# Kernel optimization log

Measured on AMD Instinct MI355X. Metric: run time of the kernel, lower is better.

## Reference

```python
import jax, jax.numpy as jnp
import numpy as np

B, M, N, P, H, W, D, DIMG, NH = 32, 2048, 512, 16, 640, 640, 256, 384, 8
PD = 3 * P * P  # 768 flattened patch dim


def layer_norm(x, g, b, eps=1e-5):
    mu = x.mean(-1, keepdims=True)
    var = ((x - mu) ** 2).mean(-1, keepdims=True)
    return (x - mu) * jax.lax.rsqrt(var + eps) * g + b


def get_patches(img, kpts, patch):
    # img [B,3,H,W], kpts [B,N,2] (x,y), NaN rows -> NaN patches
    Bb, C, Hh, Ww = img.shape
    half = patch // 2
    safe = jnp.nan_to_num(kpts, nan=0.0)
    ctr = jnp.round(safe).astype(jnp.int32)
    x0 = jnp.clip(ctr[..., 0] - half, 0, Ww - patch)
    y0 = jnp.clip(ctr[..., 1] - half, 0, Hh - patch)
    offs = jnp.arange(patch)
    ys = y0[..., None] + offs  # [B,N,P]
    xs = x0[..., None] + offs  # [B,N,P]

    def ext(im_b, ys_b, xs_b):
        p = im_b[:, ys_b[:, :, None], xs_b[:, None, :]]  # [C,N,P,P]
        return jnp.transpose(p, (1, 0, 2, 3))  # [N,C,P,P]

    patches = jax.vmap(ext)(img, ys, xs)  # [B,N,C,P,P]
    invalid = jnp.isnan(kpts).any(-1)
    return jnp.where(invalid[:, :, None, None, None], jnp.nan, patches)


def setup_inputs() -> dict:
    key = jax.random.key(0)
    ks = jax.random.split(key, 16)
    im0 = jax.random.uniform(ks[0], (B, 3, H, W), jnp.float32)
    im1 = jax.random.uniform(ks[1], (B, 3, H, W), jnp.float32)
    wh = jnp.array([W - 1.0, H - 1.0], jnp.float32)
    kpts0 = jax.random.uniform(ks[2], (B, M, 2), jnp.float32) * wh
    kpts1 = jax.random.uniform(ks[3], (B, M, 2), jnp.float32) * wh
    scores0 = jax.random.uniform(ks[4], (B, M), jnp.float32)
    scores1 = jax.random.uniform(ks[5], (B, M), jnp.float32)
    image_embs = jax.random.normal(ks[6], (B, DIMG), jnp.float32)
    m0 = jax.random.randint(ks[7], (B, N), 0, M)
    m1 = jax.random.randint(ks[8], (B, N), -300, M)
    m1 = jnp.where(m1 < 0, -1, m1)
    sorted_matches = jnp.stack([m0, m1], axis=-1).astype(jnp.int32)
    s = 0.02
    params = dict(
        ln1_g=jnp.ones((PD,), jnp.float32), ln1_b=jnp.zeros((PD,), jnp.float32),
        W_pe=jax.random.normal(ks[9], (D - 1, PD), jnp.float32) * s,
        b_pe=jnp.zeros((D - 1,), jnp.float32),
        ln2_g=jnp.ones((D - 1,), jnp.float32), ln2_b=jnp.zeros((D - 1,), jnp.float32),
        W_proj=jax.random.normal(ks[10], (D, DIMG), jnp.float32) * s,
        b_proj=jnp.zeros((D,), jnp.float32),
        in_w=jax.random.normal(ks[11], (3 * D, D), jnp.float32) * s,
        in_b=jnp.zeros((3 * D,), jnp.float32),
        out_w=jax.random.normal(ks[12], (D, D), jnp.float32) * s,
        out_b=jnp.zeros((D,), jnp.float32),
        W_fc=jax.random.normal(ks[13], (6, D), jnp.float32) * s,
        b_fc=jnp.zeros((6,), jnp.float32),
    )
    return dict(im0=im0, im1=im1, kpts0=kpts0, kpts1=kpts1, scores0=scores0,
                scores1=scores1, image_embs=image_embs,
                sorted_matches=sorted_matches, **params)


def reference(im0, im1, kpts0, kpts1, scores0, scores1, image_embs,
              sorted_matches, ln1_g, ln1_b, W_pe, b_pe, ln2_g, ln2_b,
              W_proj, b_proj, in_w, in_b, out_w, out_b, W_fc, b_fc):
    im0 = jnp.clip(im0, 0.0, 1.0)
    im1 = jnp.clip(im1, 0.0, 1.0)
    m0 = sorted_matches[..., 0]
    m1 = sorted_matches[..., 1]
    valid = m1 > -1  # [B,N]
    m0c = jnp.clip(m0, 0, M - 1)
    m1c = jnp.clip(m1, 0, M - 1)
    # vectorized masked gather with NaN padding (replaces the double python loop)
    g0 = jnp.take_along_axis(kpts0, m0c[..., None], axis=1)  # [B,N,2]
    g1 = jnp.take_along_axis(kpts1, m1c[..., None], axis=1)
    k0v = jnp.where(valid[..., None], g0, jnp.nan)
    k1v = jnp.where(valid[..., None], g1, jnp.nan)
    s0v = jnp.where(valid, jnp.take_along_axis(scores0, m0c, axis=1), 0.0)
    s1v = jnp.where(valid, jnp.take_along_axis(scores1, m1c, axis=1), 0.0)
    p0 = jnp.nan_to_num(get_patches(im0, k0v, P), nan=-1.0)  # [B,N,3,P,P]
    p1 = jnp.nan_to_num(get_patches(im1, k1v, P), nan=-1.0)
    patches = jnp.concatenate([p0, p1], axis=1)  # [B,2N,3,P,P]
    flat = patches.reshape(B, 2 * N, PD)
    e = layer_norm(flat, ln1_g, ln1_b)
    e = e @ W_pe.T + b_pe
    e = layer_norm(e, ln2_g, ln2_b)  # [B,2N,D-1]
    scores = jnp.concatenate([s0v, s1v], axis=1)  # [B,2N]
    pe = jnp.concatenate([e, scores[..., None]], axis=-1)  # [B,2N,D]
    # motion estimator: cross-attn, query = projected image embedding
    q = image_embs @ W_proj.T + b_proj  # [B,D]
    Wq, Wk, Wv = in_w[:D], in_w[D:2 * D], in_w[2 * D:]
    bq, bk, bv = in_b[:D], in_b[D:2 * D], in_b[2 * D:]
    dh = D // NH
    qh = (q @ Wq.T + bq).reshape(B, 1, NH, dh)
    kh = (pe @ Wk.T + bk).reshape(B, 2 * N, NH, dh)
    vh = (pe @ Wv.T + bv).reshape(B, 2 * N, NH, dh)
    scale = 1.0 / np.sqrt(dh).astype(np.float32)
    att = jnp.einsum('bqhd,bkhd->bhqk', qh, kh) * scale
    a = jax.nn.softmax(att, axis=-1)
    o = jnp.einsum('bhqk,bkhd->bqhd', a, vh).reshape(B, 1, D)
    o = o @ out_w.T + out_b
    out = (o @ W_fc.T + b_fc).reshape(B, 6)
    return out
```

## Files before the change

### kernel.cpp

```cpp
#include <hip/hip_runtime.h>
#include <math.h>

#define BB 32
#define MM 2048
#define NN 512
#define PSZ 16
#define HH 640
#define WW 640
#define DD 256
#define DIMG_ 384
#define NHEADS 8
#define PD_ 768
#define TWO_N 1024
#define ROWS_TOT (BB * TWO_N)
#define CHCT 32

typedef short bf16x8 __attribute__((ext_vector_type(8)));
typedef float f32x4  __attribute__((ext_vector_type(4)));

__device__ __forceinline__ unsigned short f2bf(float x) {
  unsigned int u = __float_as_uint(x);
  u = (u + 0x7FFF + ((u >> 16) & 1)) >> 16;
  return (unsigned short)u;
}
__device__ __forceinline__ float bf2f(unsigned short h) {
  return __uint_as_float(((unsigned int)h) << 16);
}

__device__ __forceinline__ void gload_lds16(const void* g, void* l) {
  __builtin_amdgcn_global_load_lds(
      (const __attribute__((address_space(1))) void*)g,
      (__attribute__((address_space(3))) void*)l, 16, 0, 0);
}

__global__ __launch_bounds__(256) void prep_extract_kernel(
    const float* __restrict__ W_pe,
    unsigned short* __restrict__ Whi, unsigned short* __restrict__ Wlo,
    const float* __restrict__ image_embs,
    const float* __restrict__ W_proj, const float* __restrict__ b_proj,
    const float* __restrict__ in_w,   const float* __restrict__ in_b,
    float* __restrict__ u_out, float* __restrict__ bias_out,
    const float* __restrict__ im0, const float* __restrict__ im1,
    const float* __restrict__ kpts0, const float* __restrict__ kpts1,
    const float* __restrict__ scores0, const float* __restrict__ scores1,
    const int*   __restrict__ sorted_matches,
    const float* __restrict__ ln1_g, const float* __restrict__ ln1_b,
    unsigned short* __restrict__ Ahi, unsigned short* __restrict__ Alo,
    float* __restrict__ score_all)
{
  __shared__ float q1[DD];
  __shared__ float q2[DD];
  const int t = threadIdx.x;

  if (blockIdx.x < 768) {
    const int idx = blockIdx.x * 256 + t;
    const int row = idx / PD_;
    float v = (row < 255) ? W_pe[idx] : 0.0f;
    const unsigned short h = f2bf(v);
    Whi[idx] = h;
    Wlo[idx] = f2bf(v - bf2f(h));
    return;
  }

  if (blockIdx.x < 800) {
    const int b = blockIdx.x - 768;
    {
      const float4* emb = (const float4*)(image_embs + (size_t)b * DIMG_);
      const float4* wr  = (const float4*)(W_proj + (size_t)t * DIMG_);
      float a = b_proj[t];
      #pragma unroll 4
      for (int i = 0; i < DIMG_ / 4; ++i) {
        const float4 e4 = emb[i], w4 = wr[i];
        a += e4.x * w4.x + e4.y * w4.y + e4.z * w4.z + e4.w * w4.w;
      }
      q1[t] = a;
    }
    __syncthreads();
    {
      const float4* wr = (const float4*)(in_w + (size_t)t * DD);
      const float4* qq = (const float4*)q1;
      float a = in_b[t];
      #pragma unroll 4
      for (int i = 0; i < DD / 4; ++i) {
        const float4 q4 = qq[i], w4 = wr[i];
        a += q4.x * w4.x + q4.y * w4.y + q4.z * w4.z + q4.w * w4.w;
      }
      q2[t] = a;
    }
    __syncthreads();
    #pragma unroll
    for (int h = 0; h < NHEADS; ++h) {
      float s = 0.0f;
      #pragma unroll 8
      for (int i = 0; i < 32; ++i)
        s += q2[h * 32 + i] * in_w[(size_t)(DD + h * 32 + i) * DD + t];
      u_out[((size_t)b * NHEADS + h) * DD + t] = s;
    }
    if (t < NHEADS) {
      float s = 0.0f;
      for (int i = 0; i < 32; ++i) s += q2[t * 32 + i] * in_b[DD + t * 32 + i];
      bias_out[b * NHEADS + t] = s;
    }
    return;
  }

  const int L  = t & 63;
  const long gp = (long)(blockIdx.x - 800) * 4 + (t >> 6);
  const int b   = (int)(gp >> 10);
  const int n2  = (int)(gp & 1023);
  const bool side1 = (n2 >= NN);
  const float* img  = side1 ? im1 : im0;
  const float* kpts = side1 ? kpts1 : kpts0;
  const float* scrs = side1 ? scores1 : scores0;

  const int n  = side1 ? (n2 - NN) : n2;
  const int m0 = sorted_matches[((size_t)b * NN + n) * 2 + 0];
  const int m1 = sorted_matches[((size_t)b * NN + n) * 2 + 1];
  const bool valid = (m1 > -1);
  int midx = side1 ? m1 : m0;
  midx = min(max(midx, 0), MM - 1);
  const float kx = kpts[((size_t)b * MM + midx) * 2 + 0];
  const float ky = kpts[((size_t)b * MM + midx) * 2 + 1];
  const int x0 = min(max((int)rintf(kx) - 8, 0), WW - PSZ);
  const int y0 = min(max((int)rintf(ky) - 8, 0), HH - PSZ);

  float v[12];
  if (valid) {
    const size_t imb = (size_t)b * 3 * HH * WW;
    const int px = (2 * L) & 15;
    #pragma unroll
    for (int j = 0; j < 6; ++j) {
      const int p0 = 2 * L + 128 * j;
      const int c  = p0 >> 8;
      const int py = (p0 >> 4) & 15;
      const float* rp = img + imb + ((size_t)c * HH + y0 + py) * WW + x0 + px;
      v[2 * j]     = fminf(fmaxf(rp[0], 0.0f), 1.0f);
      v[2 * j + 1] = fminf(fmaxf(rp[1], 0.0f), 1.0f);
    }
  } else {
    #pragma unroll
    for (int i = 0; i < 12; ++i) v[i] = -1.0f;
  }

  float s = 0.0f, ss = 0.0f;
  #pragma unroll
  for (int i = 0; i < 12; ++i) { s += v[i]; ss += v[i] * v[i]; }
  #pragma unroll
  for (int m = 32; m; m >>= 1) { s += __shfl_xor(s, m); ss += __shfl_xor(ss, m); }
  const float mu  = s * (1.0f / 768.0f);
  const float var = ss * (1.0f / 768.0f) - mu * mu;
  const float rs  = 1.0f / sqrtf(var + 1e-5f);

  unsigned int* AhiW = (unsigned int*)(Ahi + gp * PD_);
  unsigned int* AloW = (unsigned int*)(Alo + gp * PD_);
  #pragma unroll
  for (int j = 0; j < 6; ++j) {
    const int p0 = 2 * L + 128 * j;
    const float y0e = (v[2 * j]     - mu) * rs * ln1_g[p0]     + ln1_b[p0];
    const float y1e = (v[2 * j + 1] - mu) * rs * ln1_g[p0 + 1] + ln1_b[p0 + 1];
    const unsigned short h0 = f2bf(y0e), h1 = f2bf(y1e);
    AhiW[p0 >> 1] = (unsigned int)h0 | ((unsigned int)h1 << 16);
    const unsigned short l0 = f2bf(y0e - bf2f(h0));
    const unsigned short l1 = f2bf(y1e - bf2f(h1));
    AloW[p0 >> 1] = (unsigned int)l0 | ((unsigned int)l1 << 16);
  }
  if (L == 0) {
    score_all[gp] = valid ? scrs[(size_t)b * MM + midx] : 0.0f;
  }
}

__global__ __launch_bounds__(256, 2) void gemm_fused_kernel(
    const unsigned short* __restrict__ Ahi, const unsigned short* __restrict__ Alo,
    const unsigned short* __restrict__ Whi, const unsigned short* __restrict__ Wlo,
    const float* __restrict__ b_pe,
    const float* __restrict__ ln2_g, const float* __restrict__ ln2_b,
    const float* __restrict__ score_all,
    float* __restrict__ pe)
{
  __shared__ __align__(16) unsigned short sm[20480];
  const int t = threadIdx.x;
  const int w = t >> 6, L = t & 63;
  const int mt = blockIdx.x;

  const int rr   = L >> 2;
  const int q_st = (L & 3) ^ ((L >> 4) & 3);
  const int lane_m = L & 15, quad = L >> 4;
  const int swz = quad ^ (lane_m >> 2);

  const unsigned short* gsrc[10];
  int ldst[10];
  #pragma unroll
  for (int c = 0; c < 10; ++c) {
    const int cc = w + 4 * c;
    const unsigned short* sp; long rb; int dst;
    if (cc < 4)       { sp = Ahi; rb = (long)mt * 64 + cc * 16;       dst = cc * 512; }
    else if (cc < 8)  { sp = Alo; rb = (long)mt * 64 + (cc - 4) * 16; dst = 2048 + (cc - 4) * 512; }
    else if (cc < 24) { sp = Whi; rb = (long)(cc - 8) * 16;           dst = 4096 + (cc - 8) * 512; }
    else              { sp = Wlo; rb = (long)(cc - 24) * 16;          dst = 12288 + (cc - 24) * 512; }
    gsrc[c] = sp + (rb + rr) * (long)PD_ + q_st * 8;
    ldst[c] = dst;
  }

  f32x4 acc[4][4];
  #pragma unroll
  for (int i = 0; i < 4; ++i)
    #pragma unroll
    for (int j = 0; j < 4; ++j) acc[i][j] = (f32x4){0.f, 0.f, 0.f, 0.f};

  for (int ks = 0; ks < PD_ / 32; ++ks) {
    const int k0 = ks * 32;
    __syncthreads();
    #pragma unroll
    for (int c = 0; c < 10; ++c)
      gload_lds16(gsrc[c] + k0, sm + ldst[c]);
    __syncthreads();

    bf16x8 ah[4], al[4];
    #pragma unroll
    for (int i = 0; i < 4; ++i) {
      const int offa = (i * 16 + lane_m) * 32 + swz * 8;
      ah[i] = *(const bf16x8*)(sm + offa);
      al[i] = *(const bf16x8*)(sm + 2048 + offa);
    }
    #pragma unroll
    for (int j = 0; j < 4; ++j) {
      const int offb = (w * 64 + j * 16 + lane_m) * 32 + swz * 8;
      const bf16x8 bh = *(const bf16x8*)(sm + 4096 + offb);
      const bf16x8 bl = *(const bf16x8*)(sm + 12288 + offb);
      #pragma unroll
      for (int i = 0; i < 4; ++i) {
        acc[i][j] = __builtin_amdgcn_mfma_f32_16x16x32_bf16(ah[i], bh, acc[i][j], 0, 0, 0);
        acc[i][j] = __builtin_amdgcn_mfma_f32_16x16x32_bf16(ah[i], bl, acc[i][j], 0, 0, 0);
        acc[i][j] = __builtin_amdgcn_mfma_f32_16x16x32_bf16(al[i], bh, acc[i][j], 0, 0, 0);
      }
    }
  }

  __syncthreads();
  float* const fs = (float*)sm;
  float p4[4], g4[4], b4[4];
  #pragma unroll
  for (int j = 0; j < 4; ++j) {
    const int c = w * 64 + j * 16 + lane_m;
    const bool cv = (c < 255);
    p4[j] = cv ? b_pe[c]  : 0.0f;
    g4[j] = cv ? ln2_g[c] : 0.0f;
    b4[j] = cv ? ln2_b[c] : 0.0f;
  }
  float sv[16], qv[16];
  #pragma unroll
  for (int i = 0; i < 4; ++i)
    #pragma unroll
    for (int v = 0; v < 4; ++v) {
      float s = 0.0f, q = 0.0f;
      #pragma unroll
      for (int j = 0; j < 4; ++j) {
        const float x = acc[i][j][v] + p4[j];
        s += x; q += x * x;
      }
      sv[i * 4 + v] = s; qv[i * 4 + v] = q;
    }
  #pragma unroll
  for (int iv = 0; iv < 16; ++iv) {
    #pragma unroll
    for (int m = 1; m <= 8; m <<= 1) {
      sv[iv] += __shfl_xor(sv[iv], m);
      qv[iv] += __shfl_xor(qv[iv], m);
    }
  }
  if (lane_m == 0) {
    #pragma unroll
    for (int i = 0; i < 4; ++i)
      #pragma unroll
      for (int v = 0; v < 4; ++v) {
        const int row = i * 16 + quad * 4 + v;
        fs[w * 64 + row]       = sv[i * 4 + v];
        fs[256 + w * 64 + row] = qv[i * 4 + v];
      }
  }
  __syncthreads();
  if (t < 64) {
    const float S  = fs[t] + fs[64 + t] + fs[128 + t] + fs[192 + t];
    const float SS = fs[256 + t] + fs[320 + t] + fs[384 + t] + fs[448 + t];
    const float mu  = S * (1.0f / 255.0f);
    const float var = SS * (1.0f / 255.0f) - mu * mu;
    fs[512 + t] = mu;
    fs[576 + t] = 1.0f / sqrtf(var + 1e-5f);
  }
  __syncthreads();

  #pragma unroll
  for (int i = 0; i < 4; ++i)
    #pragma unroll
    for (int v = 0; v < 4; ++v) {
      const int row = i * 16 + quad * 4 + v;
      const long grow = (long)mt * 64 + row;
      const float mu = fs[512 + row];
      const float rs = fs[576 + row];
      float sc = 0.0f;
      if (w == 3) sc = score_all[grow];
      float* rowp = pe + grow * DD + w * 64 + lane_m;
      #pragma unroll
      for (int j = 0; j < 4; ++j) {
        const int c = w * 64 + j * 16 + lane_m;
        const float y = (c < 255)
            ? (acc[i][j][v] + p4[j] - mu) * rs * g4[j] + b4[j]
            : sc;
        rowp[j * 16] = y;
      }
    }
}

__global__ __launch_bounds__(256) void logits_kernel(
    const float* __restrict__ pe,
    const float* __restrict__ u, const float* __restrict__ ubias,
    float* __restrict__ lt)
{
  __shared__ __align__(16) float u_sh[NHEADS * DD];
  __shared__ float ub_sh[NHEADS];
  const int t = threadIdx.x;
  const long row0 = (long)blockIdx.x * 8;
  const int b = (int)(row0 >> 10);

  const float* ub = u + (size_t)b * NHEADS * DD;
  #pragma unroll
  for (int i = 0; i < 8; ++i) u_sh[t + 256 * i] = ub[t + 256 * i];
  if (t < NHEADS) ub_sh[t] = ubias[b * NHEADS + t];
  __syncthreads();

  const int r = t >> 5, l = t & 31;
  const long row = row0 + r;
  const float4* pr4 = (const float4*)(pe + row * DD);
  float d[NHEADS] = {0, 0, 0, 0, 0, 0, 0, 0};
  #pragma unroll
  for (int half = 0; half < 2; ++half) {
    const float4 x = pr4[l + 32 * half];
    #pragma unroll
    for (int h = 0; h < NHEADS; ++h) {
      const float4 uu = *(const float4*)&u_sh[h * DD + 4 * (l + 32 * half)];
      d[h] += x.x * uu.x + x.y * uu.y + x.z * uu.z + x.w * uu.w;
    }
  }
  #pragma unroll
  for (int h = 0; h < NHEADS; ++h) {
    #pragma unroll
    for (int m = 16; m; m >>= 1) d[h] += __shfl_xor(d[h], m, 32);
  }
  if (l == 0) {
    #pragma unroll
    for (int h = 0; h < NHEADS; ++h)
      lt[row * NHEADS + h] = (d[h] + ub_sh[h]) * 0.17677669529663687f;
  }
}

__global__ __launch_bounds__(256) void softmax_kernel(
    const float* __restrict__ lt, float* __restrict__ prg)
{
  const int b = blockIdx.x, t = threadIdx.x;
  const int h = t >> 5, l = t & 31;
  const float* base = lt + (size_t)b * TWO_N * NHEADS + h;
  float v[32];
  float mx = -1e30f;
  #pragma unroll 8
  for (int i = 0; i < 32; ++i) { v[i] = base[(l + 32 * i) * NHEADS]; mx = fmaxf(mx, v[i]); }
  #pragma unroll
  for (int m = 16; m; m >>= 1) mx = fmaxf(mx, __shfl_xor(mx, m, 32));
  float sm = 0.0f;
  #pragma unroll 8
  for (int i = 0; i < 32; ++i) { v[i] = expf(v[i] - mx); sm += v[i]; }
  #pragma unroll
  for (int m = 16; m; m >>= 1) sm += __shfl_xor(sm, m, 32);
  const float inv = 1.0f / sm;
  float* out = prg + (size_t)b * TWO_N * NHEADS + h;
  #pragma unroll 8
  for (int i = 0; i < 32; ++i) out[(l + 32 * i) * NHEADS] = v[i] * inv;
}

__global__ __launch_bounds__(256) void ctx_kernel(
    const float* __restrict__ pe, const float* __restrict__ prg,
    float* __restrict__ ctxp)
{
  __shared__ __align__(16) float prc[32 * NHEADS];
  const int b = blockIdx.x, ch = blockIdx.y, t = threadIdx.x;
  prc[t] = prg[((size_t)b * TWO_N + ch * 32) * NHEADS + t];
  __syncthreads();

  const float* peb = pe + ((size_t)b * TWO_N + ch * 32) * DD;
  float acc[NHEADS] = {0, 0, 0, 0, 0, 0, 0, 0};
  #pragma unroll 4
  for (int k = 0; k < 32; ++k) {
    const float v = peb[(size_t)k * DD + t];
    const float4 a0 = *(const float4*)&prc[k * NHEADS];
    const float4 a1 = *(const float4*)&prc[k * NHEADS + 4];
    acc[0] += a0.x * v; acc[1] += a0.y * v; acc[2] += a0.z * v; acc[3] += a0.w * v;
    acc[4] += a1.x * v; acc[5] += a1.y * v; acc[6] += a1.z * v; acc[7] += a1.w * v;
  }
  #pragma unroll
  for (int h = 0; h < NHEADS; ++h)
    ctxp[(((size_t)b * CHCT + ch) * NHEADS + h) * DD + t] = acc[h];
}

__global__ __launch_bounds__(256) void final_kernel(
    const float* __restrict__ ctxp,
    const float* __restrict__ in_w,  const float* __restrict__ in_b,
    const float* __restrict__ out_w, const float* __restrict__ out_b,
    const float* __restrict__ W_fc,  const float* __restrict__ b_fc,
    float* __restrict__ outp)
{
  __shared__ __align__(16) float ctx_sh[NHEADS * DD];
  __shared__ __align__(16) float o_sh[DD], o2_sh[DD];
  const int t = threadIdx.x;
  const int b = blockIdx.x;

  #pragma unroll
  for (int h = 0; h < NHEADS; ++h) {
    float s = 0.0f;
    #pragma unroll
    for (int ch = 0; ch < CHCT; ++ch)
      s += ctxp[(((size_t)b * CHCT + ch) * NHEADS + h) * DD + t];
    ctx_sh[h * DD + t] = s;
  }
  __syncthreads();
  {
    const float4* wv = (const float4*)(in_w + (size_t)(2 * DD + t) * DD);
    const float4* cx = (const float4*)(ctx_sh + (t >> 5) * DD);
    float o1 = in_b[2 * DD + t];
    #pragma unroll 4
    for (int j = 0; j < DD / 4; ++j) {
      const float4 w4 = wv[j], c4 = cx[j];
      o1 += w4.x * c4.x + w4.y * c4.y + w4.z * c4.z + w4.w * c4.w;
    }
    o_sh[t] = o1;
  }
  __syncthreads();
  {
    const float4* wr = (const float4*)(out_w + (size_t)t * DD);
    const float4* oo = (const float4*)o_sh;
    float o2 = out_b[t];
    #pragma unroll 4
    for (int j = 0; j < DD / 4; ++j) {
      const float4 w4 = wr[j], c4 = oo[j];
      o2 += w4.x * c4.x + w4.y * c4.y + w4.z * c4.z + w4.w * c4.w;
    }
    o2_sh[t] = o2;
  }
  __syncthreads();
  if (t < 6) {
    const float4* wr = (const float4*)(W_fc + (size_t)t * DD);
    const float4* oo = (const float4*)o2_sh;
    float r = b_fc[t];
    for (int j = 0; j < DD / 4; ++j) {
      const float4 w4 = wr[j], c4 = oo[j];
      r += w4.x * c4.x + w4.y * c4.y + w4.z * c4.z + w4.w * c4.w;
    }
    outp[b * 6 + t] = r;
  }
}

extern "C" void kernel_launch(void* const* d_in, const int* in_sizes, int n_in,
                              void* d_out, int out_size, void* d_ws, size_t ws_size,
                              hipStream_t stream) {
  const float* im0       = (const float*)d_in[0];
  const float* im1       = (const float*)d_in[1];
  const float* kpts0     = (const float*)d_in[2];
  const float* kpts1     = (const float*)d_in[3];
  const float* scores0   = (const float*)d_in[4];
  const float* scores1   = (const float*)d_in[5];
  const float* image_embs= (const float*)d_in[6];
  const int*   smatch    = (const int*)d_in[7];
  const float* ln1_g     = (const float*)d_in[8];
  const float* ln1_b     = (const float*)d_in[9];
  const float* W_pe      = (const float*)d_in[10];
  const float* b_pe      = (const float*)d_in[11];
  const float* ln2_g     = (const float*)d_in[12];
  const float* ln2_b     = (const float*)d_in[13];
  const float* W_proj    = (const float*)d_in[14];
  const float* b_proj    = (const float*)d_in[15];
  const float* in_w      = (const float*)d_in[16];
  const float* in_b      = (const float*)d_in[17];
  const float* out_w     = (const float*)d_in[18];
  const float* out_b     = (const float*)d_in[19];
  const float* W_fc      = (const float*)d_in[20];
  const float* b_fc      = (const float*)d_in[21];

  char* ws = (char*)d_ws;
  size_t off = 0;
  float* epe   = (float*)(ws + off); off += (size_t)ROWS_TOT * DD * 4;
  float* u     = (float*)(ws + off); off += (size_t)BB * NHEADS * DD * 4;
  float* ubias = (float*)(ws + off); off += (size_t)BB * NHEADS * 4;
  off = (off + 1023) & ~(size_t)1023;
  float* score = (float*)(ws + off); off += (size_t)ROWS_TOT * 4;
  float* lt    = (float*)(ws + off); off += (size_t)BB * TWO_N * NHEADS * 4;
  float* prg   = (float*)(ws + off); off += (size_t)BB * TWO_N * NHEADS * 4;
  float* ctxp  = (float*)(ws + off); off += (size_t)BB * CHCT * NHEADS * DD * 4;
  off = (off + 1023) & ~(size_t)1023;
  unsigned short* Whi = (unsigned short*)(ws + off); off += (size_t)256 * PD_ * 2;
  unsigned short* Wlo = (unsigned short*)(ws + off); off += (size_t)256 * PD_ * 2;
  off = (off + 1023) & ~(size_t)1023;
  unsigned short* Ahi = (unsigned short*)(ws + off); off += (size_t)ROWS_TOT * PD_ * 2;
  unsigned short* Alo = (unsigned short*)(ws + off); off += (size_t)ROWS_TOT * PD_ * 2;

  prep_extract_kernel<<<800 + ROWS_TOT / 4, 256, 0, stream>>>(
      W_pe, Whi, Wlo, image_embs, W_proj, b_proj, in_w, in_b, u, ubias,
      im0, im1, kpts0, kpts1, scores0, scores1, smatch,
      ln1_g, ln1_b, Ahi, Alo, score);
  gemm_fused_kernel<<<ROWS_TOT / 64, 256, 0, stream>>>(
      Ahi, Alo, Whi, Wlo, b_pe, ln2_g, ln2_b, score, epe);
  logits_kernel<<<ROWS_TOT / 8, 256, 0, stream>>>(epe, u, ubias, lt);
  softmax_kernel<<<BB, 256, 0, stream>>>(lt, prg);
  ctx_kernel<<<dim3(BB, CHCT), 256, 0, stream>>>(epe, prg, ctxp);
  final_kernel<<<BB, 256, 0, stream>>>(ctxp, in_w, in_b, out_w, out_b,
                                       W_fc, b_fc, (float*)d_out);
}
```

Baseline: 473.1 us.

## Double-buffer GEMM LDS tiles and vectorize patch gather with float4 loads

The bf16x3 GEMM main loop now ping-pongs between two LDS buffers. It issues the global-to-LDS copy of the next K-slice before computing on the current one, which leaves one barrier per iteration instead of two. This doubles the kernel's shared memory and relaxes the launch-bounds occupancy hint, so fewer blocks may fit per CU. Separately, the patch extraction kernel now maps each lane to a row and a 4-pixel column group, loading 16 bytes per channel and writing packed 8-byte hi/lo bf16 stores, with vectorized LayerNorm gamma and beta loads.

```diff
diff --git a/kernel.cpp b/kernel.cpp
--- a/kernel.cpp
+++ b/kernel.cpp
@@ -124,18 +124,21 @@
   const int x0 = min(max((int)rintf(kx) - 8, 0), WW - PSZ);
   const int y0 = min(max((int)rintf(ky) - 8, 0), HH - PSZ);
 
+  const int r4 = L >> 2;
+  const int q4 = L & 3;
+
   float v[12];
   if (valid) {
     const size_t imb = (size_t)b * 3 * HH * WW;
-    const int px = (2 * L) & 15;
-    #pragma unroll
-    for (int j = 0; j < 6; ++j) {
-      const int p0 = 2 * L + 128 * j;
-      const int c  = p0 >> 8;
-      const int py = (p0 >> 4) & 15;
-      const float* rp = img + imb + ((size_t)c * HH + y0 + py) * WW + x0 + px;
-      v[2 * j]     = fminf(fmaxf(rp[0], 0.0f), 1.0f);
-      v[2 * j + 1] = fminf(fmaxf(rp[1], 0.0f), 1.0f);
+    const float* rbase = img + imb + (size_t)(y0 + r4) * WW + x0 + 4 * q4;
+    #pragma unroll
+    for (int c = 0; c < 3; ++c) {
+      float4 f;
+      __builtin_memcpy(&f, rbase + (size_t)c * HH * WW, 16);
+      v[4 * c + 0] = fminf(fmaxf(f.x, 0.0f), 1.0f);
+      v[4 * c + 1] = fminf(fmaxf(f.y, 0.0f), 1.0f);
+      v[4 * c + 2] = fminf(fmaxf(f.z, 0.0f), 1.0f);
+      v[4 * c + 3] = fminf(fmaxf(f.w, 0.0f), 1.0f);
     }
   } else {
     #pragma unroll
@@ -151,25 +154,34 @@
   const float var = ss * (1.0f / 768.0f) - mu * mu;
   const float rs  = 1.0f / sqrtf(var + 1e-5f);
 
-  unsigned int* AhiW = (unsigned int*)(Ahi + gp * PD_);
-  unsigned int* AloW = (unsigned int*)(Alo + gp * PD_);
-  #pragma unroll
-  for (int j = 0; j < 6; ++j) {
-    const int p0 = 2 * L + 128 * j;
-    const float y0e = (v[2 * j]     - mu) * rs * ln1_g[p0]     + ln1_b[p0];
-    const float y1e = (v[2 * j + 1] - mu) * rs * ln1_g[p0 + 1] + ln1_b[p0 + 1];
+  const int p0base = r4 * 16 + q4 * 4;
+  unsigned short* const ahr = Ahi + gp * PD_;
+  unsigned short* const alr = Alo + gp * PD_;
+  #pragma unroll
+  for (int c = 0; c < 3; ++c) {
+    const int p0 = c * 256 + p0base;
+    const float4 gv = *(const float4*)(ln1_g + p0);
+    const float4 bv = *(const float4*)(ln1_b + p0);
+    const float y0e = (v[4 * c + 0] - mu) * rs * gv.x + bv.x;
+    const float y1e = (v[4 * c + 1] - mu) * rs * gv.y + bv.y;
+    const float y2e = (v[4 * c + 2] - mu) * rs * gv.z + bv.z;
+    const float y3e = (v[4 * c + 3] - mu) * rs * gv.w + bv.w;
     const unsigned short h0 = f2bf(y0e), h1 = f2bf(y1e);
-    AhiW[p0 >> 1] = (unsigned int)h0 | ((unsigned int)h1 << 16);
-    const unsigned short l0 = f2bf(y0e - bf2f(h0));
-    const unsigned short l1 = f2bf(y1e - bf2f(h1));
-    AloW[p0 >> 1] = (unsigned int)l0 | ((unsigned int)l1 << 16);
+    const unsigned short h2 = f2bf(y2e), h3 = f2bf(y3e);
+    uint2 hw, lw;
+    hw.x = (unsigned int)h0 | ((unsigned int)h1 << 16);
+    hw.y = (unsigned int)h2 | ((unsigned int)h3 << 16);
+    lw.x = (unsigned int)f2bf(y0e - bf2f(h0)) | ((unsigned int)f2bf(y1e - bf2f(h1)) << 16);
+    lw.y = (unsigned int)f2bf(y2e - bf2f(h2)) | ((unsigned int)f2bf(y3e - bf2f(h3)) << 16);
+    *(uint2*)(ahr + p0) = hw;
+    *(uint2*)(alr + p0) = lw;
   }
   if (L == 0) {
     score_all[gp] = valid ? scrs[(size_t)b * MM + midx] : 0.0f;
   }
 }
 
-__global__ __launch_bounds__(256, 2) void gemm_fused_kernel(
+__global__ __launch_bounds__(256) void gemm_fused_kernel(
     const unsigned short* __restrict__ Ahi, const unsigned short* __restrict__ Alo,
     const unsigned short* __restrict__ Whi, const unsigned short* __restrict__ Wlo,
     const float* __restrict__ b_pe,
@@ -177,7 +189,7 @@
     const float* __restrict__ score_all,
     float* __restrict__ pe)
 {
-  __shared__ __align__(16) unsigned short sm[20480];
+  __shared__ __align__(16) unsigned short sm[40960];
   const int t = threadIdx.x;
   const int w = t >> 6, L = t & 63;
   const int mt = blockIdx.x;
@@ -188,17 +200,18 @@
   const int swz = quad ^ (lane_m >> 2);
 
   const unsigned short* gsrc[10];
-  int ldst[10];
+  int ldst[10], bstr[10];
   #pragma unroll
   for (int c = 0; c < 10; ++c) {
     const int cc = w + 4 * c;
-    const unsigned short* sp; long rb; int dst;
-    if (cc < 4)       { sp = Ahi; rb = (long)mt * 64 + cc * 16;       dst = cc * 512; }
-    else if (cc < 8)  { sp = Alo; rb = (long)mt * 64 + (cc - 4) * 16; dst = 2048 + (cc - 4) * 512; }
-    else if (cc < 24) { sp = Whi; rb = (long)(cc - 8) * 16;           dst = 4096 + (cc - 8) * 512; }
-    else              { sp = Wlo; rb = (long)(cc - 24) * 16;          dst = 12288 + (cc - 24) * 512; }
+    const unsigned short* sp; long rb; int dst, str;
+    if (cc < 4)       { sp = Ahi; rb = (long)mt * 64 + cc * 16;       dst = cc * 512;               str = 4096;  }
+    else if (cc < 8)  { sp = Alo; rb = (long)mt * 64 + (cc - 4) * 16; dst = 2048 + (cc - 4) * 512;  str = 4096;  }
+    else if (cc < 24) { sp = Whi; rb = (long)(cc - 8) * 16;           dst = 8192 + (cc - 8) * 512;  str = 16384; }
+    else              { sp = Wlo; rb = (long)(cc - 24) * 16;          dst = 16384 + (cc - 24) * 512; str = 16384; }
     gsrc[c] = sp + (rb + rr) * (long)PD_ + q_st * 8;
     ldst[c] = dst;
+    bstr[c] = str;
   }
 
   f32x4 acc[4][4];
@@ -207,26 +220,34 @@
     #pragma unroll
     for (int j = 0; j < 4; ++j) acc[i][j] = (f32x4){0.f, 0.f, 0.f, 0.f};
 
+  #pragma unroll
+  for (int c = 0; c < 10; ++c) gload_lds16(gsrc[c], sm + ldst[c]);
+  __syncthreads();
+
+  #pragma unroll 2
   for (int ks = 0; ks < PD_ / 32; ++ks) {
-    const int k0 = ks * 32;
-    __syncthreads();
-    #pragma unroll
-    for (int c = 0; c < 10; ++c)
-      gload_lds16(gsrc[c] + k0, sm + ldst[c]);
-    __syncthreads();
+    const int p = ks & 1;
+    if (ks < PD_ / 32 - 1) {
+      const int k0n = (ks + 1) * 32;
+      #pragma unroll
+      for (int c = 0; c < 10; ++c)
+        gload_lds16(gsrc[c] + k0n, sm + ldst[c] + (p ^ 1) * bstr[c]);
+    }
+    const unsigned short* Ab = sm + p * 4096;
+    const unsigned short* Bb = sm + 8192 + p * 16384;
 
     bf16x8 ah[4], al[4];
     #pragma unroll
     for (int i = 0; i < 4; ++i) {
       const int offa = (i * 16 + lane_m) * 32 + swz * 8;
-      ah[i] = *(const bf16x8*)(sm + offa);
-      al[i] = *(const bf16x8*)(sm + 2048 + offa);
+      ah[i] = *(const bf16x8*)(Ab + offa);
+      al[i] = *(const bf16x8*)(Ab + 2048 + offa);
     }
     #pragma unroll
     for (int j = 0; j < 4; ++j) {
       const int offb = (w * 64 + j * 16 + lane_m) * 32 + swz * 8;
-      const bf16x8 bh = *(const bf16x8*)(sm + 4096 + offb);
-      const bf16x8 bl = *(const bf16x8*)(sm + 12288 + offb);
+      const bf16x8 bh = *(const bf16x8*)(Bb + offb);
+      const bf16x8 bl = *(const bf16x8*)(Bb + 8192 + offb);
       #pragma unroll
       for (int i = 0; i < 4; ++i) {
         acc[i][j] = __builtin_amdgcn_mfma_f32_16x16x32_bf16(ah[i], bh, acc[i][j], 0, 0, 0);
@@ -234,9 +255,9 @@
         acc[i][j] = __builtin_amdgcn_mfma_f32_16x16x32_bf16(al[i], bh, acc[i][j], 0, 0, 0);
       }
     }
-  }
-
-  __syncthreads();
+    __syncthreads();
+  }
+
   float* const fs = (float*)sm;
   float p4[4], g4[4], b4[4];
   #pragma unroll
```

After: 476.3 us. Within noise of the previous version (+0.7%).
